# Kernel optimization log

Hardware: AMD Instinct MI355X
Metric: run time of the kernel (lower is better)

The kernel has to match this reference:

```python
import jax, jax.numpy as jnp
import numpy as np

N = 50000          # nodes
E = 800000         # edges (avg in-degree 16)
F = 128            # hidden_dim
AVG_LOG = float(np.log(17.0))  # PyG avg_deg['log'] from deg histogram concentrated at degree 16
BN_EPS = 1e-5
STD_EPS = 1e-5


def setup_inputs() -> dict:
    key = jax.random.key(0)
    ks = jax.random.split(key, 10)
    h = jax.random.normal(ks[0], (N, F), dtype=jnp.float32)
    edge_index = jax.random.randint(ks[1], (2, E), 0, N, dtype=jnp.int64)

    def lin_w(k, fan_in, fan_out):
        return jax.random.normal(k, (fan_in, fan_out), dtype=jnp.float32) / np.sqrt(fan_in)

    return {
        "h": h,
        "edge_index": edge_index,
        "W_pre": lin_w(ks[2], 2 * F, F),   # pre_nn: Linear(2F -> F) on [x_i, x_j]
        "b_pre": jnp.zeros((F,), jnp.float32),
        "W_post": lin_w(ks[3], 13 * F, F),  # post_nn: Linear((1 + 4*3)F -> F)
        "b_post": jnp.zeros((F,), jnp.float32),
        "W_lin": lin_w(ks[4], F, F),       # final Linear(F -> F)
        "b_lin": jnp.zeros((F,), jnp.float32),
        "gamma": jnp.ones((F,), jnp.float32),   # BatchNorm1d weight
        "beta": jnp.zeros((F,), jnp.float32),   # BatchNorm1d bias
    }


def reference(h, edge_index, W_pre, b_pre, W_post, b_post, W_lin, b_lin, gamma, beta):
    src = edge_index[0]  # x_j (message source)
    dst = edge_index[1]  # x_i (aggregation target)
    n = h.shape[0]

    # pre_nn on concat([x_i, x_j])  -> per-edge message [E, F]
    m = jnp.concatenate([h[dst], h[src]], axis=-1) @ W_pre + b_pre

    # multi-aggregator scatter: mean, min, max, std (PyG order)
    cnt = jax.ops.segment_sum(jnp.ones((m.shape[0],), m.dtype), dst, num_segments=n)  # [N]
    deg = jnp.maximum(cnt, 1.0)[:, None]                                              # clamp(1)
    mean = jax.ops.segment_sum(m, dst, num_segments=n) / deg
    mean_sq = jax.ops.segment_sum(m * m, dst, num_segments=n) / deg
    std = jnp.sqrt(jax.nn.relu(mean_sq - mean * mean) + STD_EPS)
    has = (cnt > 0)[:, None]
    mn = jnp.where(has, jax.ops.segment_min(m, dst, num_segments=n), 0.0)
    mx = jnp.where(has, jax.ops.segment_max(m, dst, num_segments=n), 0.0)
    aggr = jnp.concatenate([mean, mn, mx, std], axis=-1)  # [N, 4F]

    # degree scalers: identity, amplification, attenuation
    logd = jnp.log(deg + 1.0)
    out = jnp.concatenate(
        [aggr, aggr * (logd / AVG_LOG), aggr * (AVG_LOG / logd)], axis=-1
    )  # [N, 12F]

    # update: concat self features, post_nn, final lin
    out = jnp.concatenate([h, out], axis=-1) @ W_post + b_post  # [N, F]
    out = out @ W_lin + b_lin

    # BatchNorm1d (training-mode batch statistics, biased variance) + ReLU
    mu = out.mean(axis=0)
    var = out.var(axis=0)
    out = (out - mu) / jnp.sqrt(var + BN_EPS) * gamma + beta
    out = jax.nn.relu(out)
    # dropout p=0.0 is identity; residual add
    return out + h
```

## Files before the change

### kernel.cpp

```cpp
#include <hip/hip_runtime.h>
#include <hip/hip_bf16.h>
#include <cstdint>
#include <cstddef>

typedef short s16x8 __attribute__((ext_vector_type(8)));
typedef float f32x4 __attribute__((ext_vector_type(4)));

#define AVG_LOG_F 2.8332133f

static __device__ __forceinline__ float b2f(unsigned short u) {
  union { unsigned int i; float f; } x; x.i = ((unsigned int)u) << 16; return x.f;
}
static __device__ __forceinline__ unsigned short f2b(float f) {
  __hip_bfloat16 h = __float2bfloat16(f);
  union { __hip_bfloat16 hh; unsigned short u; } c; c.hh = h; return c.u;
}
static __device__ __forceinline__ unsigned int pack2(float lo, float hi) {
  return (unsigned int)f2b(lo) | ((unsigned int)f2b(hi) << 16);
}
static __device__ __forceinline__ int swz(int row, int slot) {
  return row * 32 + ((slot ^ ((row >> 1) & 3)) << 3);
}

__global__ void conv_h_kernel(const float* __restrict__ h, unsigned short* __restrict__ hb, int total4) {
  int i = blockIdx.x * blockDim.x + threadIdx.x;
  if (i >= total4) return;
  const float4 v = ((const float4*)h)[i];
  uint2 r;
  r.x = pack2(v.x, v.y);
  r.y = pack2(v.z, v.w);
  ((uint2*)hb)[i] = r;
}

__global__ void fold_wcat_kernel(const float* __restrict__ W_pre, unsigned short* __restrict__ WcatT) {
  int idx = blockIdx.x * blockDim.x + threadIdx.x;
  int c = idx >> 7, k = idx & 127;
  float v = (c < 128) ? W_pre[k * 128 + c] : W_pre[(128 + k) * 128 + (c - 128)];
  WcatT[c * 128 + k] = f2b(v);
}

__global__ __launch_bounds__(128) void fold_wpost_kernel(
    const float* __restrict__ W_post, const float* __restrict__ b_post,
    const float* __restrict__ W_lin, const float* __restrict__ b_lin,
    unsigned short* __restrict__ WfoldT, float* __restrict__ bfold) {
  __shared__ float wl[128 * 128];
  const int j = threadIdx.x;
  for (int r = 0; r < 128; ++r) wl[r * 128 + j] = W_lin[r * 128 + j];
  __syncthreads();
  if (blockIdx.x == 208) {
    float acc = b_lin[j];
    for (int k = 0; k < 128; ++k) acc += b_post[k] * wl[k * 128 + j];
    bfold[j] = acc;
  } else {
#pragma unroll 2
    for (int ii = 0; ii < 8; ++ii) {
      const int i = blockIdx.x * 8 + ii;
      float acc = 0.f;
      for (int k = 0; k < 128; ++k) acc += W_post[i * 128 + k] * wl[k * 128 + j];
      WfoldT[(size_t)j * 1664 + i] = f2b(acc);
    }
  }
}

__global__ void bucket_hist_kernel(const int* __restrict__ dst, int* __restrict__ bucketCnt, int E) {
  __shared__ int lcnt[256];
  const int tid = threadIdx.x;
  lcnt[tid] = 0;
  __syncthreads();
  for (int e = blockIdx.x * 256 + tid; e < E; e += gridDim.x * 256)
    atomicAdd(&lcnt[dst[e] >> 8], 1);
  __syncthreads();
  if (lcnt[tid] > 0) atomicAdd(&bucketCnt[tid], lcnt[tid]);
}

__global__ void bucket_scan_kernel(const int* __restrict__ bucketCnt, int* __restrict__ bucketBase,
                                   int* __restrict__ bucketCursor, int* __restrict__ rowptr,
                                   int n, int nb, int E) {
  __shared__ int sh[256];
  const int tid = threadIdx.x;
  const int v = (tid < nb) ? bucketCnt[tid] : 0;
  sh[tid] = v;
  __syncthreads();
  for (int o = 1; o < 256; o <<= 1) {
    int t = (tid >= o) ? sh[tid - o] : 0;
    __syncthreads();
    sh[tid] += t;
    __syncthreads();
  }
  const int base = sh[tid] - v;
  if (tid < nb) { bucketBase[tid] = base; bucketCursor[tid] = base; }
  if (tid == nb - 1) bucketBase[nb] = base + v;
  if (tid == 0) rowptr[n] = E;
}

__global__ __launch_bounds__(256) void s1_scatter_kernel(
    const int* __restrict__ src, const int* __restrict__ dst,
    int* __restrict__ bucketCursor, unsigned int* __restrict__ bucketed, int E, int CH) {
  __shared__ int lcnt[256], loff[256], lcur[256], gbase[256];
  __shared__ unsigned int stage[5000];
  __shared__ unsigned char sbid[5000];
  const int tid = threadIdx.x;
  const int c0 = blockIdx.x * CH;
  const int c1 = min(c0 + CH, E);
  const int cnt = c1 - c0;
  if (cnt <= 0) return;
  lcnt[tid] = 0;
  __syncthreads();
  for (int e = c0 + tid; e < c1; e += 256) atomicAdd(&lcnt[dst[e] >> 8], 1);
  __syncthreads();
  const int v = lcnt[tid];
  loff[tid] = 0;
  __syncthreads();
  {
    __shared__ int tmp[256];
    tmp[tid] = v;
    __syncthreads();
    for (int o = 1; o < 256; o <<= 1) {
      int t = (tid >= o) ? tmp[tid - o] : 0;
      __syncthreads();
      tmp[tid] += t;
      __syncthreads();
    }
    loff[tid] = tmp[tid] - v;
  }
  lcur[tid] = loff[tid];
  gbase[tid] = (v > 0) ? atomicAdd(&bucketCursor[tid], v) : 0;
  __syncthreads();
  for (int e = c0 + tid; e < c1; e += 256) {
    const int d = dst[e];
    const int b = d >> 8;
    const int slot = atomicAdd(&lcur[b], 1);
    stage[slot] = ((unsigned int)(d & 255) << 16) | (unsigned int)src[e];
    sbid[slot] = (unsigned char)b;
  }
  __syncthreads();
  for (int i = tid; i < cnt; i += 256) {
    const int b = sbid[i];
    bucketed[gbase[b] + (i - loff[b])] = stage[i];
  }
}

__global__ __launch_bounds__(256) void s2_build_kernel(
    const unsigned int* __restrict__ bucketed, const int* __restrict__ bucketBase,
    int* __restrict__ rowptr, unsigned short* __restrict__ ssrc, int n) {
  __shared__ int ncnt[256], noff[256], ncur[256];
  __shared__ unsigned short csr16[8192];
  const int tid = threadIdx.x;
  const int b = blockIdx.x;
  const int seg0 = bucketBase[b], seg1 = bucketBase[b + 1];
  const int cnt = seg1 - seg0;
  ncnt[tid] = 0;
  __syncthreads();
  for (int i = tid; i < cnt; i += 256) atomicAdd(&ncnt[bucketed[seg0 + i] >> 16], 1);
  __syncthreads();
  const int v = ncnt[tid];
  {
    __shared__ int tmp[256];
    tmp[tid] = v;
    __syncthreads();
    for (int o = 1; o < 256; o <<= 1) {
      int t = (tid >= o) ? tmp[tid - o] : 0;
      __syncthreads();
      tmp[tid] += t;
      __syncthreads();
    }
    noff[tid] = tmp[tid] - v;
  }
  ncur[tid] = noff[tid];
  const int node = (b << 8) + tid;
  if (node < n) rowptr[node] = seg0 + noff[tid];
  __syncthreads();
  for (int i = tid; i < cnt; i += 256) {
    const unsigned int rec = bucketed[seg0 + i];
    const int d = rec >> 16;
    const int slot = atomicAdd(&ncur[d], 1);
    if (slot < 8192) csr16[slot] = (unsigned short)(rec & 0xffffu);
  }
  __syncthreads();
  for (int i = tid; i < cnt; i += 256) ssrc[seg0 + i] = csr16[i];
}

__global__ __launch_bounds__(256) void gemm256_kernel(
    const unsigned short* __restrict__ A, const unsigned short* __restrict__ BT,
    unsigned short* __restrict__ outb, int M)
{
  constexpr int LDT = 40;
  constexpr int K = 128, NK = K / 32;
  __shared__ alignas(16) unsigned short Asm[2][128 * LDT];
  __shared__ alignas(16) unsigned short Bsm[2][128 * LDT];
  const int tid = threadIdx.x, lane = tid & 63;
  const int w = tid >> 6, wr = w >> 1, wc = w & 1;
  const int row0 = blockIdx.x * 128;
  const int col0 = blockIdx.y * 128;
  const int srow = tid >> 2, slot = tid & 3;
  const int ar0 = min(row0 + srow, M - 1);
  const int ar1 = min(row0 + srow + 64, M - 1);
  const unsigned short* ap0 = A + (size_t)ar0 * K + slot * 8;
  const unsigned short* ap1 = A + (size_t)ar1 * K + slot * 8;
  const unsigned short* bp0 = BT + (size_t)(col0 + srow) * K + slot * 8;
  const unsigned short* bp1 = BT + (size_t)(col0 + srow + 64) * K + slot * 8;
  const int wa0 = srow * LDT + slot * 8, wa1 = wa0 + 64 * LDT;

  int offA[4], offB[4];
#pragma unroll
  for (int i = 0; i < 4; ++i) {
    offA[i] = (wr * 64 + i * 16 + (lane & 15)) * LDT + (lane >> 4) * 8;
    offB[i] = (wc * 64 + i * 16 + (lane & 15)) * LDT + (lane >> 4) * 8;
  }

  f32x4 acc[4][4] = {};
  uint4 a0 = *(const uint4*)ap0;
  uint4 a1 = *(const uint4*)ap1;
  uint4 b0 = *(const uint4*)bp0;
  uint4 b1 = *(const uint4*)bp1;
  *(uint4*)&Asm[0][wa0] = a0; *(uint4*)&Asm[0][wa1] = a1;
  *(uint4*)&Bsm[0][wa0] = b0; *(uint4*)&Bsm[0][wa1] = b1;
  __syncthreads();

  for (int kt = 0; kt < NK; ++kt) {
    const int cur = kt & 1;
    if (kt + 1 < NK) {
      const int k0 = (kt + 1) * 32;
      a0 = *(const uint4*)(ap0 + k0); a1 = *(const uint4*)(ap1 + k0);
      b0 = *(const uint4*)(bp0 + k0); b1 = *(const uint4*)(bp1 + k0);
    }
    s16x8 af[4], bq[4];
#pragma unroll
    for (int i = 0; i < 4; ++i) af[i] = *(const s16x8*)&Asm[cur][offA[i]];
#pragma unroll
    for (int i = 0; i < 4; ++i) bq[i] = *(const s16x8*)&Bsm[cur][offB[i]];
#pragma unroll
    for (int mi = 0; mi < 4; ++mi)
#pragma unroll
      for (int ni = 0; ni < 4; ++ni)
        acc[mi][ni] = __builtin_amdgcn_mfma_f32_16x16x32_bf16(af[mi], bq[ni], acc[mi][ni], 0, 0, 0);
    if (kt + 1 < NK) {
      const int nxt = cur ^ 1;
      *(uint4*)&Asm[nxt][wa0] = a0; *(uint4*)&Asm[nxt][wa1] = a1;
      *(uint4*)&Bsm[nxt][wa0] = b0; *(uint4*)&Bsm[nxt][wa1] = b1;
      __syncthreads();
    }
  }

#pragma unroll
  for (int mi = 0; mi < 4; ++mi) {
#pragma unroll
    for (int ni = 0; ni < 4; ++ni) {
      const int rbase = row0 + wr * 64 + mi * 16 + (lane >> 4) * 4;
      const int c = col0 + wc * 64 + ni * 16 + (lane & 15);
#pragma unroll
      for (int r = 0; r < 4; ++r) {
        const int rr = rbase + r;
        if (rr < M) outb[(size_t)rr * 256 + c] = f2b(acc[mi][ni][r]);
      }
    }
  }
}

#define AGG_EDGE(IDX)                                                                  \
  {                                                                                    \
    const unsigned int v = *(const unsigned int*)(AB + (size_t)(IDX) * 256 + 128 + 2 * lane); \
    const float v0 = b2f((unsigned short)(v & 0xffffu));                               \
    const float v1 = b2f((unsigned short)(v >> 16));                                   \
    s0 += v0; q0 += v0 * v0; mn0 = fminf(mn0, v0); mx0 = fmaxf(mx0, v0);               \
    s1v += v1; q1 += v1 * v1; mn1 = fminf(mn1, v1); mx1 = fmaxf(mx1, v1);              \
  }

__global__ void aggregate_kernel(const unsigned short* __restrict__ AB,
                                 const unsigned short* __restrict__ hb,
                                 const float* __restrict__ b_pre,
                                 const int* __restrict__ rowptr, const unsigned short* __restrict__ ssrc,
                                 unsigned short* __restrict__ Xagg,
                                 float* __restrict__ sc1, float* __restrict__ sc2, int n) {
  const int node = blockIdx.x * 4 + (threadIdx.x >> 6);
  if (node >= n) return;
  const int lane = threadIdx.x & 63;
  const int beg = rowptr[node], end = rowptr[node + 1];
  const int cnt = end - beg;
  float s0 = 0.f, s1v = 0.f, q0 = 0.f, q1 = 0.f;
  float mn0 = 3.4e38f, mn1 = 3.4e38f, mx0 = -3.4e38f, mx1 = -3.4e38f;
  for (int base = beg; base < end; base += 64) {
    const int m = min(64, end - base);
    const int myidx = (base + lane < end) ? (int)ssrc[base + lane] : 0;
    int t = 0;
    for (; t + 8 <= m; t += 8) {
      const int i0 = __builtin_amdgcn_readlane(myidx, t + 0);
      const int i1 = __builtin_amdgcn_readlane(myidx, t + 1);
      const int i2 = __builtin_amdgcn_readlane(myidx, t + 2);
      const int i3 = __builtin_amdgcn_readlane(myidx, t + 3);
      const int i4 = __builtin_amdgcn_readlane(myidx, t + 4);
      const int i5 = __builtin_amdgcn_readlane(myidx, t + 5);
      const int i6 = __builtin_amdgcn_readlane(myidx, t + 6);
      const int i7 = __builtin_amdgcn_readlane(myidx, t + 7);
      AGG_EDGE(i0) AGG_EDGE(i1) AGG_EDGE(i2) AGG_EDGE(i3)
      AGG_EDGE(i4) AGG_EDGE(i5) AGG_EDGE(i6) AGG_EDGE(i7)
    }
    for (; t < m; ++t) {
      const int i0 = __builtin_amdgcn_readlane(myidx, t);
      AGG_EDGE(i0)
    }
  }
  const float degf = (float)(cnt > 0 ? cnt : 1);
  const float2 bp = ((const float2*)b_pre)[lane];
  const unsigned int cpair = *(const unsigned int*)(AB + (size_t)node * 256 + 2 * lane);
  const float c0 = b2f((unsigned short)(cpair & 0xffffu)) + bp.x;
  const float c1 = b2f((unsigned short)(cpair >> 16)) + bp.y;
  float mean0, mean1, std0, std1, lo0, lo1, hi0, hi1;
  if (cnt > 0) {
    const float inv = 1.f / degf;
    const float mu0 = s0 * inv, mu1 = s1v * inv;
    mean0 = c0 + mu0; mean1 = c1 + mu1;
    std0 = sqrtf(fmaxf(q0 * inv - mu0 * mu0, 0.f) + 1e-5f);
    std1 = sqrtf(fmaxf(q1 * inv - mu1 * mu1, 0.f) + 1e-5f);
    lo0 = c0 + mn0; lo1 = c1 + mn1; hi0 = c0 + mx0; hi1 = c1 + mx1;
  } else {
    mean0 = mean1 = lo0 = lo1 = hi0 = hi1 = 0.f;
    std0 = std1 = sqrtf(1e-5f);
  }
  const float logd = logf(degf + 1.f);
  unsigned int* row = (unsigned int*)(Xagg + (size_t)node * 640);
  row[lane]       = *(const unsigned int*)(hb + (size_t)node * 128 + 2 * lane);
  row[64 + lane]  = pack2(mean0, mean1);
  row[128 + lane] = pack2(lo0, lo1);
  row[192 + lane] = pack2(hi0, hi1);
  row[256 + lane] = pack2(std0, std1);
  if (lane == 0) { sc1[node] = logd / AVG_LOG_F; sc2[node] = AVG_LOG_F / logd; }
}

static __device__ __forceinline__ uint4 scale8(uint4 r, float s) {
  union { uint4 v; unsigned short h[8]; } in, out;
  in.v = r;
#pragma unroll
  for (int i = 0; i < 8; ++i) out.h[i] = f2b(b2f(in.h[i]) * s);
  return out.v;
}
static __device__ __forceinline__ uint4 loadA_fold(const unsigned short* base, int kc,
                                                   float s1v, float s2v) {
  const bool m1 = kc >= 640;
  const bool m2 = kc >= 1152;
  const int off = kc - (m1 ? 512 : 0) - (m2 ? 512 : 0);
  uint4 r = *(const uint4*)(base + off);
  if (m1) r = scale8(r, m2 ? s2v : s1v);
  return r;
}

__global__ __launch_bounds__(512) void gemm_fold2_kernel(
    const unsigned short* __restrict__ Xagg, const float* __restrict__ sc1,
    const float* __restrict__ sc2, const unsigned short* __restrict__ WT,
    const float* __restrict__ bias, float* __restrict__ out3,
    float* __restrict__ bnsum, int M)
{
  constexpr int NK = 52;
  __shared__ alignas(16) unsigned short Asm[2][128 * 32];
  __shared__ alignas(16) unsigned short Bsm[2][128 * 32];
  __shared__ float bnacc[256];
  const int tid = threadIdx.x, lane = tid & 63, w = tid >> 6;
  const int wr = w >> 2, wc = w & 3;
  const int row0 = blockIdx.x * 128;
  const int srow = tid >> 2, slot = tid & 3;
  const int arow = min(row0 + srow, M - 1);
  const unsigned short* abase = Xagg + (size_t)arow * 640;
  const unsigned short* bbase = WT + (size_t)srow * 1664 + slot * 8;
  const float s1v = sc1[arow], s2v = sc2[arow];
  const int wa = swz(srow, slot);
  if (tid < 256) bnacc[tid] = 0.f;

  int offA[4], offB[2];
#pragma unroll
  for (int i = 0; i < 4; ++i) offA[i] = swz(wr * 64 + i * 16 + (lane & 15), lane >> 4);
#pragma unroll
  for (int i = 0; i < 2; ++i) offB[i] = swz(wc * 32 + i * 16 + (lane & 15), lane >> 4);

  f32x4 acc[4][2] = {};
  uint4 a = loadA_fold(abase, slot * 8, s1v, s2v);
  uint4 b = *(const uint4*)bbase;
  *(uint4*)&Asm[0][wa] = a;
  *(uint4*)&Bsm[0][wa] = b;
  __syncthreads();

  for (int kt = 0; kt < NK; ++kt) {
    const int cur = kt & 1;
    const bool pf = kt + 1 < NK;
    if (pf) {
      const int kc = (kt + 1) * 32 + slot * 8;
      a = loadA_fold(abase, kc, s1v, s2v);
      b = *(const uint4*)(bbase + (kt + 1) * 32);
    }
    s16x8 af[4], bq[2];
#pragma unroll
    for (int i = 0; i < 4; ++i) af[i] = *(const s16x8*)&Asm[cur][offA[i]];
#pragma unroll
    for (int i = 0; i < 2; ++i) bq[i] = *(const s16x8*)&Bsm[cur][offB[i]];
#pragma unroll
    for (int mi = 0; mi < 4; ++mi)
#pragma unroll
      for (int ni = 0; ni < 2; ++ni)
        acc[mi][ni] = __builtin_amdgcn_mfma_f32_16x16x32_bf16(af[mi], bq[ni], acc[mi][ni], 0, 0, 0);
    if (pf) {
      const int nxt = cur ^ 1;
      *(uint4*)&Asm[nxt][wa] = a;
      *(uint4*)&Bsm[nxt][wa] = b;
      __syncthreads();
    }
  }

  float cs[2] = {0.f, 0.f}, css[2] = {0.f, 0.f};
#pragma unroll
  for (int mi = 0; mi < 4; ++mi) {
#pragma unroll
    for (int ni = 0; ni < 2; ++ni) {
      const int rbase = row0 + wr * 64 + mi * 16 + (lane >> 4) * 4;
      const int c = wc * 32 + ni * 16 + (lane & 15);
      const float bb = bias[c];
#pragma unroll
      for (int r = 0; r < 4; ++r) {
        const int rr = rbase + r;
        if (rr < M) {
          const float v = acc[mi][ni][r] + bb;
          out3[(size_t)rr * 128 + c] = v;
          cs[ni] += v; css[ni] += v * v;
        }
      }
    }
  }
  __syncthreads();
#pragma unroll
  for (int ni = 0; ni < 2; ++ni) {
    const int c = wc * 32 + ni * 16 + (lane & 15);
    atomicAdd(&bnacc[c], cs[ni]);
    atomicAdd(&bnacc[128 + c], css[ni]);
  }
  __syncthreads();
  if (tid < 128) {
    atomicAdd(&bnsum[tid], bnacc[tid]);
    atomicAdd(&bnsum[128 + tid], bnacc[128 + tid]);
  }
}

__global__ void bnfinal_kernel(const float* __restrict__ bnsum, const float* __restrict__ gamma,
                               const float* __restrict__ beta, float* __restrict__ sc,
                               float* __restrict__ shv, int n) {
  const int f = threadIdx.x;
  const float inv = 1.f / (float)n;
  const float mu = bnsum[f] * inv;
  const float var = bnsum[128 + f] * inv - mu * mu;
  const float rstd = rsqrtf(var + 1e-5f);
  const float s = gamma[f] * rstd;
  sc[f] = s;
  shv[f] = beta[f] - mu * s;
}

__global__ void epilogue_kernel(const float* __restrict__ out3, const float* __restrict__ h,
                                const float* __restrict__ sc, const float* __restrict__ shv,
                                float* __restrict__ out, int total4) {
  int i = blockIdx.x * blockDim.x + threadIdx.x;
  if (i >= total4) return;
  const int c = (i & 31) * 4;
  const float4 x = ((const float4*)out3)[i];
  const float4 hh = ((const float4*)h)[i];
  float4 r;
  r.x = fmaxf(x.x * sc[c + 0] + shv[c + 0], 0.f) + hh.x;
  r.y = fmaxf(x.y * sc[c + 1] + shv[c + 1], 0.f) + hh.y;
  r.z = fmaxf(x.z * sc[c + 2] + shv[c + 2], 0.f) + hh.z;
  r.w = fmaxf(x.w * sc[c + 3] + shv[c + 3], 0.f) + hh.w;
  ((float4*)out)[i] = r;
}

extern "C" void kernel_launch(void* const* d_in, const int* in_sizes, int n_in,
                              void* d_out, int out_size, void* d_ws, size_t ws_size,
                              hipStream_t stream) {
  const float* h      = (const float*)d_in[0];
  const int*   ei     = (const int*)d_in[1];
  const float* W_pre  = (const float*)d_in[2];
  const float* b_pre  = (const float*)d_in[3];
  const float* W_post = (const float*)d_in[4];
  const float* b_post = (const float*)d_in[5];
  const float* W_lin  = (const float*)d_in[6];
  const float* b_lin  = (const float*)d_in[7];
  const float* gamma  = (const float*)d_in[8];
  const float* beta   = (const float*)d_in[9];

  const int n = in_sizes[0] / 128;
  const int E = in_sizes[1] / 2;
  const int* src = ei;
  const int* dst = ei + E;

  char* ws = (char*)d_ws;
  size_t off = 0;
  auto carve = [&](size_t bytes) {
    off = (off + 255) & ~(size_t)255;
    void* p = ws + off;
    off += bytes;
    return p;
  };
  unsigned short* hb   = (unsigned short*)carve((size_t)n * 128 * 2);
  void* ab_out3        = carve((size_t)n * 256 * 2);
  unsigned short* AB   = (unsigned short*)ab_out3;
  float* out3          = (float*)ab_out3;
  unsigned short* Xagg = (unsigned short*)carve((size_t)n * 640 * 2);
  float* sc1           = (float*)carve((size_t)n * 4);
  float* sc2           = (float*)carve((size_t)n * 4);
  unsigned short* WcatT  = (unsigned short*)carve(256 * 128 * 2);
  unsigned short* WfoldT = (unsigned short*)carve((size_t)128 * 1664 * 2);
  float* bfold         = (float*)carve(128 * 4);
  int*   bucketCnt     = (int*)carve(256 * 4);
  int*   bucketBase    = (int*)carve(257 * 4);
  int*   bucketCursor  = (int*)carve(256 * 4);
  unsigned int* bucketed = (unsigned int*)carve((size_t)E * 4);
  int*   rowptr        = (int*)carve((size_t)(n + 1) * 4);
  unsigned short* ssrc = (unsigned short*)carve((size_t)(E + 2) * 2);
  float* bnsum         = (float*)carve(256 * 4);
  float* bnsc          = (float*)carve(128 * 4);
  float* bnsh          = (float*)carve(128 * 4);

  const int total4 = n * 128 / 4;
  const int mt = (n + 127) / 128;
  const int nb = (n + 255) >> 8;
  const int nS1 = (E + 4999) / 5000;

  conv_h_kernel<<<(total4 + 255) / 256, 256, 0, stream>>>(h, hb, total4);
  fold_wcat_kernel<<<128, 256, 0, stream>>>(W_pre, WcatT);
  fold_wpost_kernel<<<209, 128, 0, stream>>>(W_post, b_post, W_lin, b_lin, WfoldT, bfold);

  hipMemsetAsync(bucketCnt, 0, 256 * 4, stream);
  hipMemsetAsync(bnsum, 0, 256 * 4, stream);
  bucket_hist_kernel<<<256, 256, 0, stream>>>(dst, bucketCnt, E);
  bucket_scan_kernel<<<1, 256, 0, stream>>>(bucketCnt, bucketBase, bucketCursor, rowptr, n, nb, E);
  s1_scatter_kernel<<<nS1, 256, 0, stream>>>(src, dst, bucketCursor, bucketed, E, 5000);
  s2_build_kernel<<<nb, 256, 0, stream>>>(bucketed, bucketBase, rowptr, ssrc, n);

  gemm256_kernel<<<dim3(mt, 2), 256, 0, stream>>>(hb, WcatT, AB, n);
  aggregate_kernel<<<(n + 3) / 4, 256, 0, stream>>>(AB, hb, b_pre, rowptr, ssrc, Xagg, sc1, sc2, n);
  gemm_fold2_kernel<<<mt, 512, 0, stream>>>(Xagg, sc1, sc2, WfoldT, bfold, out3, bnsum, n);

  bnfinal_kernel<<<1, 128, 0, stream>>>(bnsum, gamma, beta, bnsc, bnsh, n);
  epilogue_kernel<<<(total4 + 255) / 256, 256, 0, stream>>>(out3, h, bnsc, bnsh, (float*)d_out, total4);
}
```

Baseline: 299.1 us.

## Fuse fp32-to-bf16 conversion into consumers, fold BN finalize into epilogue, restructure fold GEMM

Removes the separate h-to-bf16 conversion kernel: gemm256 now loads fp32 h and converts it while staging into shared memory, and aggregate packs h directly. The single-block BN finalize kernel is folded into the epilogue, which recomputes per-feature scale and shift from the accumulated sums. The fold GEMM main loop is unrolled by two, with explicit double-register prefetch so loads run a further stage ahead. These cut two launches and one intermediate buffer round trip, at the cost of reading twice as many bytes for the A operand in gemm256 and doing redundant rsqrt work per element in the epilogue.

```diff
diff --git a/kernel.cpp b/kernel.cpp
--- a/kernel.cpp
+++ b/kernel.cpp
@@ -18,18 +18,16 @@
 static __device__ __forceinline__ unsigned int pack2(float lo, float hi) {
   return (unsigned int)f2b(lo) | ((unsigned int)f2b(hi) << 16);
 }
+static __device__ __forceinline__ uint4 cvt8(const float* p) {
+  const float4 lo = *(const float4*)p;
+  const float4 hi = *(const float4*)(p + 4);
+  uint4 r;
+  r.x = pack2(lo.x, lo.y); r.y = pack2(lo.z, lo.w);
+  r.z = pack2(hi.x, hi.y); r.w = pack2(hi.z, hi.w);
+  return r;
+}
 static __device__ __forceinline__ int swz(int row, int slot) {
   return row * 32 + ((slot ^ ((row >> 1) & 3)) << 3);
-}
-
-__global__ void conv_h_kernel(const float* __restrict__ h, unsigned short* __restrict__ hb, int total4) {
-  int i = blockIdx.x * blockDim.x + threadIdx.x;
-  if (i >= total4) return;
-  const float4 v = ((const float4*)h)[i];
-  uint2 r;
-  r.x = pack2(v.x, v.y);
-  r.y = pack2(v.z, v.w);
-  ((uint2*)hb)[i] = r;
 }
 
 __global__ void fold_wcat_kernel(const float* __restrict__ W_pre, unsigned short* __restrict__ WcatT) {
@@ -181,7 +179,7 @@
 }
 
 __global__ __launch_bounds__(256) void gemm256_kernel(
-    const unsigned short* __restrict__ A, const unsigned short* __restrict__ BT,
+    const float* __restrict__ A, const unsigned short* __restrict__ BT,
     unsigned short* __restrict__ outb, int M)
 {
   constexpr int LDT = 40;
@@ -195,8 +193,8 @@
   const int srow = tid >> 2, slot = tid & 3;
   const int ar0 = min(row0 + srow, M - 1);
   const int ar1 = min(row0 + srow + 64, M - 1);
-  const unsigned short* ap0 = A + (size_t)ar0 * K + slot * 8;
-  const unsigned short* ap1 = A + (size_t)ar1 * K + slot * 8;
+  const float* ap0 = A + (size_t)ar0 * K + slot * 8;
+  const float* ap1 = A + (size_t)ar1 * K + slot * 8;
   const unsigned short* bp0 = BT + (size_t)(col0 + srow) * K + slot * 8;
   const unsigned short* bp1 = BT + (size_t)(col0 + srow + 64) * K + slot * 8;
   const int wa0 = srow * LDT + slot * 8, wa1 = wa0 + 64 * LDT;
@@ -209,8 +207,8 @@
   }
 
   f32x4 acc[4][4] = {};
-  uint4 a0 = *(const uint4*)ap0;
-  uint4 a1 = *(const uint4*)ap1;
+  uint4 a0 = cvt8(ap0);
+  uint4 a1 = cvt8(ap1);
   uint4 b0 = *(const uint4*)bp0;
   uint4 b1 = *(const uint4*)bp1;
   *(uint4*)&Asm[0][wa0] = a0; *(uint4*)&Asm[0][wa1] = a1;
@@ -221,7 +219,7 @@
     const int cur = kt & 1;
     if (kt + 1 < NK) {
       const int k0 = (kt + 1) * 32;
-      a0 = *(const uint4*)(ap0 + k0); a1 = *(const uint4*)(ap1 + k0);
+      a0 = cvt8(ap0 + k0); a1 = cvt8(ap1 + k0);
       b0 = *(const uint4*)(bp0 + k0); b1 = *(const uint4*)(bp1 + k0);
     }
     s16x8 af[4], bq[4];
@@ -267,7 +265,7 @@
   }
 
 __global__ void aggregate_kernel(const unsigned short* __restrict__ AB,
-                                 const unsigned short* __restrict__ hb,
+                                 const float* __restrict__ h,
                                  const float* __restrict__ b_pre,
                                  const int* __restrict__ rowptr, const unsigned short* __restrict__ ssrc,
                                  unsigned short* __restrict__ Xagg,
@@ -318,8 +316,9 @@
     std0 = std1 = sqrtf(1e-5f);
   }
   const float logd = logf(degf + 1.f);
+  const float2 hv = ((const float2*)(h + (size_t)node * 128))[lane];
   unsigned int* row = (unsigned int*)(Xagg + (size_t)node * 640);
-  row[lane]       = *(const unsigned int*)(hb + (size_t)node * 128 + 2 * lane);
+  row[lane]       = pack2(hv.x, hv.y);
   row[64 + lane]  = pack2(mean0, mean1);
   row[128 + lane] = pack2(lo0, lo1);
   row[192 + lane] = pack2(hi0, hi1);
@@ -343,6 +342,19 @@
   if (m1) r = scale8(r, m2 ? s2v : s1v);
   return r;
 }
+
+#define FOLD_MFMA(CUR)                                                              \
+  {                                                                                 \
+    s16x8 af[4], bq[2];                                                             \
+    _Pragma("unroll") for (int i = 0; i < 4; ++i)                                   \
+        af[i] = *(const s16x8*)&Asm[CUR][offA[i]];                                  \
+    _Pragma("unroll") for (int i = 0; i < 2; ++i)                                   \
+        bq[i] = *(const s16x8*)&Bsm[CUR][offB[i]];                                  \
+    _Pragma("unroll") for (int mi = 0; mi < 4; ++mi)                                \
+      _Pragma("unroll") for (int ni = 0; ni < 2; ++ni)                              \
+        acc[mi][ni] = __builtin_amdgcn_mfma_f32_16x16x32_bf16(af[mi], bq[ni],       \
+                                                              acc[mi][ni], 0, 0, 0);\
+  }
 
 __global__ __launch_bounds__(512) void gemm_fold2_kernel(
     const unsigned short* __restrict__ Xagg, const float* __restrict__ sc1,
@@ -372,35 +384,37 @@
   for (int i = 0; i < 2; ++i) offB[i] = swz(wc * 32 + i * 16 + (lane & 15), lane >> 4);
 
   f32x4 acc[4][2] = {};
-  uint4 a = loadA_fold(abase, slot * 8, s1v, s2v);
-  uint4 b = *(const uint4*)bbase;
-  *(uint4*)&Asm[0][wa] = a;
-  *(uint4*)&Bsm[0][wa] = b;
-  __syncthreads();
-
-  for (int kt = 0; kt < NK; ++kt) {
-    const int cur = kt & 1;
-    const bool pf = kt + 1 < NK;
-    if (pf) {
-      const int kc = (kt + 1) * 32 + slot * 8;
-      a = loadA_fold(abase, kc, s1v, s2v);
-      b = *(const uint4*)(bbase + (kt + 1) * 32);
-    }
-    s16x8 af[4], bq[2];
-#pragma unroll
-    for (int i = 0; i < 4; ++i) af[i] = *(const s16x8*)&Asm[cur][offA[i]];
-#pragma unroll
-    for (int i = 0; i < 2; ++i) bq[i] = *(const s16x8*)&Bsm[cur][offB[i]];
-#pragma unroll
-    for (int mi = 0; mi < 4; ++mi)
-#pragma unroll
-      for (int ni = 0; ni < 2; ++ni)
-        acc[mi][ni] = __builtin_amdgcn_mfma_f32_16x16x32_bf16(af[mi], bq[ni], acc[mi][ni], 0, 0, 0);
-    if (pf) {
-      const int nxt = cur ^ 1;
-      *(uint4*)&Asm[nxt][wa] = a;
-      *(uint4*)&Bsm[nxt][wa] = b;
+  {
+    uint4 a = loadA_fold(abase, slot * 8, s1v, s2v);
+    uint4 b = *(const uint4*)bbase;
+    *(uint4*)&Asm[0][wa] = a;
+    *(uint4*)&Bsm[0][wa] = b;
+  }
+  uint4 aS1 = loadA_fold(abase, 32 + slot * 8, s1v, s2v);
+  uint4 bS1 = *(const uint4*)(bbase + 32);
+  uint4 aS0, bS0;
+  __syncthreads();
+
+  for (int kt = 0; kt < NK; kt += 2) {
+    {
+      const int k2 = min(kt + 2, NK - 1) * 32;
+      aS0 = loadA_fold(abase, k2 + slot * 8, s1v, s2v);
+      bS0 = *(const uint4*)(bbase + k2);
+      FOLD_MFMA(0)
+      *(uint4*)&Asm[1][wa] = aS1;
+      *(uint4*)&Bsm[1][wa] = bS1;
       __syncthreads();
+    }
+    {
+      const int k3 = min(kt + 3, NK - 1) * 32;
+      aS1 = loadA_fold(abase, k3 + slot * 8, s1v, s2v);
+      bS1 = *(const uint4*)(bbase + k3);
+      FOLD_MFMA(1)
+      if (kt + 2 < NK) {
+        *(uint4*)&Asm[0][wa] = aS0;
+        *(uint4*)&Bsm[0][wa] = bS0;
+        __syncthreads();
+      }
     }
   }
 
@@ -437,32 +451,29 @@
   }
 }
 
-__global__ void bnfinal_kernel(const float* __restrict__ bnsum, const float* __restrict__ gamma,
-                               const float* __restrict__ beta, float* __restrict__ sc,
-                               float* __restrict__ shv, int n) {
-  const int f = threadIdx.x;
-  const float inv = 1.f / (float)n;
-  const float mu = bnsum[f] * inv;
-  const float var = bnsum[128 + f] * inv - mu * mu;
-  const float rstd = rsqrtf(var + 1e-5f);
-  const float s = gamma[f] * rstd;
-  sc[f] = s;
-  shv[f] = beta[f] - mu * s;
-}
-
 __global__ void epilogue_kernel(const float* __restrict__ out3, const float* __restrict__ h,
-                                const float* __restrict__ sc, const float* __restrict__ shv,
-                                float* __restrict__ out, int total4) {
+                                const float* __restrict__ bnsum, const float* __restrict__ gamma,
+                                const float* __restrict__ beta, float* __restrict__ out,
+                                int n, int total4) {
   int i = blockIdx.x * blockDim.x + threadIdx.x;
   if (i >= total4) return;
   const int c = (i & 31) * 4;
+  const float inv = 1.f / (float)n;
   const float4 x = ((const float4*)out3)[i];
   const float4 hh = ((const float4*)h)[i];
   float4 r;
-  r.x = fmaxf(x.x * sc[c + 0] + shv[c + 0], 0.f) + hh.x;
-  r.y = fmaxf(x.y * sc[c + 1] + shv[c + 1], 0.f) + hh.y;
-  r.z = fmaxf(x.z * sc[c + 2] + shv[c + 2], 0.f) + hh.z;
-  r.w = fmaxf(x.w * sc[c + 3] + shv[c + 3], 0.f) + hh.w;
+  float* rp = (float*)&r;
+  const float* xp = (const float*)&x;
+  const float* hp = (const float*)&hh;
+#pragma unroll
+  for (int j = 0; j < 4; ++j) {
+    const int cc = c + j;
+    const float mu = bnsum[cc] * inv;
+    const float var = bnsum[128 + cc] * inv - mu * mu;
+    const float s = gamma[cc] * rsqrtf(var + 1e-5f);
+    const float sh = beta[cc] - mu * s;
+    rp[j] = fmaxf(xp[j] * s + sh, 0.f) + hp[j];
+  }
   ((float4*)out)[i] = r;
 }
 
@@ -493,7 +504,6 @@
     off += bytes;
     return p;
   };
-  unsigned short* hb   = (unsigned short*)carve((size_t)n * 128 * 2);
   void* ab_out3        = carve((size_t)n * 256 * 2);
   unsigned short* AB   = (unsigned short*)ab_out3;
   float* out3          = (float*)ab_out3;
@@ -510,15 +520,12 @@
   int*   rowptr        = (int*)carve((size_t)(n + 1) * 4);
   unsigned short* ssrc = (unsigned short*)carve((size_t)(E + 2) * 2);
   float* bnsum         = (float*)carve(256 * 4);
-  float* bnsc          = (float*)carve(128 * 4);
-  float* bnsh          = (float*)carve(128 * 4);
 
   const int total4 = n * 128 / 4;
   const int mt = (n + 127) / 128;
   const int nb = (n + 255) >> 8;
   const int nS1 = (E + 4999) / 5000;
 
-  conv_h_kernel<<<(total4 + 255) / 256, 256, 0, stream>>>(h, hb, total4);
   fold_wcat_kernel<<<128, 256, 0, stream>>>(W_pre, WcatT);
   fold_wpost_kernel<<<209, 128, 0, stream>>>(W_post, b_post, W_lin, b_lin, WfoldT, bfold);
 
@@ -529,10 +536,10 @@
   s1_scatter_kernel<<<nS1, 256, 0, stream>>>(src, dst, bucketCursor, bucketed, E, 5000);
   s2_build_kernel<<<nb, 256, 0, stream>>>(bucketed, bucketBase, rowptr, ssrc, n);
 
-  gemm256_kernel<<<dim3(mt, 2), 256, 0, stream>>>(hb, WcatT, AB, n);
-  aggregate_kernel<<<(n + 3) / 4, 256, 0, stream>>>(AB, hb, b_pre, rowptr, ssrc, Xagg, sc1, sc2, n);
+  gemm256_kernel<<<dim3(mt, 2), 256, 0, stream>>>(h, WcatT, AB, n);
+  aggregate_kernel<<<(n + 3) / 4, 256, 0, stream>>>(AB, h, b_pre, rowptr, ssrc, Xagg, sc1, sc2, n);
   gemm_fold2_kernel<<<mt, 512, 0, stream>>>(Xagg, sc1, sc2, WfoldT, bfold, out3, bnsum, n);
 
-  bnfinal_kernel<<<1, 128, 0, stream>>>(bnsum, gamma, beta, bnsc, bnsh, n);
-  epilogue_kernel<<<(total4 + 255) / 256, 256, 0, stream>>>(out3, h, bnsc, bnsh, (float*)d_out, total4);
-}
+  epilogue_kernel<<<(total4 + 255) / 256, 256, 0, stream>>>(out3, h, bnsum, gamma, beta,
+                                                            (float*)d_out, n, total4);
+}
```

After: 287.0 us. -4.0%, faster.
